# Optimization experiments

Measured on AMD Instinct MI355X. Metric: run time of the kernel, lower is better.

The kernel has to match this reference:

```python
import jax, jax.numpy as jnp
import numpy as np

B, T, M, D, N, K = 64, 128, 256, 256, 4, 2
TEMP = 8.0  # attention_temperature


def setup_inputs() -> dict:
    key = jax.random.key(0)
    ks = jax.random.split(key, 8)
    s = 0.05
    x = jax.random.normal(ks[0], (B, T, 8), jnp.float32)
    in_W = jax.random.normal(ks[1], (D, 8), jnp.float32) * s
    in_b = jnp.zeros((D,), jnp.float32)
    out_W = jax.random.normal(ks[2], (8, D), jnp.float32) * s
    out_b = jnp.zeros((8,), jnp.float32)
    proc_W = jax.random.normal(ks[3], (1, D, D), jnp.float32) * s  # depth-1 layers
    proc_b = jnp.zeros((1, D), jnp.float32)
    dest = jax.random.uniform(ks[4], (N, M), jnp.float32) * M  # pointer_destinations
    jg_W = jax.random.normal(ks[5], (N, 1, D), jnp.float32) * s
    jg_b = jnp.zeros((N, 1), jnp.float32)
    ctx_strength = jnp.full((N,), 0.2, jnp.float32)
    PHI = 1.618033988749895
    ph = []
    for n in range(N):
        phase_v = n * PHI
        row = []
        for h in range(1, 9):
            row += [np.sin(h * phase_v), np.cos(h * phase_v)]
        ph.append(row)
    phase = jnp.asarray(np.array(ph, dtype=np.float32))  # [N,16]
    # pointer init: being n uniform in [n*M/N, (n+1)*M/N)
    lo = jnp.arange(N, dtype=jnp.float32)[:, None] * (M / N)
    ptr_init = lo + jax.random.uniform(ks[6], (N, B), jnp.float32) * (M / N)
    return dict(x=x, in_W=in_W, in_b=in_b, out_W=out_W, out_b=out_b,
                proc_W=proc_W, proc_b=proc_b, dest=dest, jg_W=jg_W, jg_b=jg_b,
                ctx_strength=ctx_strength, phase=phase, ptr_init=ptr_init)


def _forward(x, in_W, in_b, out_W, out_b, proc_W, proc_b, dest, jg_W, jg_b,
             ctx_strength, phase, ptr_init):
    offsets = jnp.arange(-K, K + 1)           # [2K+1]
    half = M / 2.0
    phase_pad = jnp.pad(phase, ((0, 0), (0, D - phase.shape[1])))  # [N,D]
    brow = jnp.arange(B)[:, None]

    def step(carry, x_t):
        ring, hid, ptr = carry                # [B,M,D], [N,B,D], [N,B]
        inp = x_t @ in_W.T + in_b             # shared input_proj: [B,D]
        outs, nh, nptr = [], [], []
        for n in range(N):                    # small fixed swarm of beings
            p = ptr[n]                        # [B]
            base = jnp.clip(jnp.floor(p), 0, M - 1).astype(jnp.int32)
            idx = (base[:, None] + offsets) % M          # [B,2K+1]
            # circular distance from window cell to fractional pointer
            delta = jnp.mod(idx.astype(p.dtype) - p[:, None] + half, M) - half
            w = jax.nn.softmax(-(delta * delta) / TEMP, axis=1)  # [B,2K+1]
            neigh = jnp.take_along_axis(ring, idx[:, :, None], axis=1)  # [B,2K+1,D]
            ctx = jnp.sum(w[:, :, None] * neigh, axis=1)  # [B,D]
            comb = inp + jax.nn.sigmoid(ctx_strength[n]) * ctx + 0.1 * phase_pad[n]
            s_ = jnp.tanh(comb + hid[n])
            for l in range(proc_W.shape[0]):
                s_ = jnp.tanh(s_ @ proc_W[l].T + proc_b[l])
            # write the new hidden state back into the shared ring (gaussian-weighted)
            ring = ring.at[brow, idx].add(w[:, :, None] * s_[:, None, :])
            # straight-through hard jump gate
            jl = (s_ @ jg_W[n].T + jg_b[n])[:, 0]        # [B]
            pr = jax.nn.sigmoid(jl)
            hard = (pr > 0.5).astype(s_.dtype)
            g = pr + jax.lax.stop_gradient(hard - pr)
            dst = dest[n][base]                           # learned jump target
            walk = jnp.mod(p + 1.0, M)
            nptr.append(jnp.mod(g * dst + (1.0 - g) * walk, M))
            outs.append(s_ @ out_W.T + out_b)             # [B,8]
            nh.append(s_)
        combined = jnp.mean(jnp.stack(outs, 0), axis=0)   # mean combiner: [B,8]
        return (ring, jnp.stack(nh, 0), jnp.stack(nptr, 0)), combined

    ring0 = jnp.zeros((B, M, D), x.dtype)
    hid0 = jnp.zeros((N, B, D), x.dtype)
    _, ys = jax.lax.scan(step, (ring0, hid0, ptr_init), jnp.swapaxes(x, 0, 1))
    return jnp.swapaxes(ys, 0, 1)                         # [B,T,8]


def reference(x, in_W, in_b, out_W, out_b, proc_W, proc_b, dest, jg_W, jg_b,
              ctx_strength, phase, ptr_init):
    return _forward(x, in_W, in_b, out_W, out_b, proc_W, proc_b, dest, jg_W,
                    jg_b, ctx_strength, phase, ptr_init)
```

## Files before the change

### kernel.cpp

```cpp
#include <hip/hip_runtime.h>
#include <hip/hip_bf16.h>
#include <math.h>

#define BB 64
#define TT 128
#define MM 256
#define DD 256
#define NB 4

__global__ __launch_bounds__(1024, 1)
void swarm_kernel(const float* __restrict__ x,
                  const float* __restrict__ in_W,
                  const float* __restrict__ in_b,
                  const float* __restrict__ out_W,
                  const float* __restrict__ out_b,
                  const float* __restrict__ proc_W,
                  const float* __restrict__ proc_b,
                  const float* __restrict__ dest,
                  const float* __restrict__ jg_W,
                  const float* __restrict__ jg_b,
                  const float* __restrict__ ctx_strength,
                  const float* __restrict__ phase,
                  const float* __restrict__ ptr_init,
                  float* __restrict__ out,
                  float* __restrict__ ws)
{
  const int b    = blockIdx.x;
  const int tid  = threadIdx.x;
  const int wave = tid >> 6;
  const int lane = tid & 63;
  const int c    = tid >> 8;
  const int jj   = tid & 255;
  const bool j256 = (tid < 256);
  const int j = tid;

  float* __restrict__ ring = ws + (size_t)b * (MM * DD);

  __shared__ __align__(16) float s_lds[DD];
  __shared__ float part_lds[4 * DD];
  __shared__ float hid_lds[NB * DD];
  __shared__ float red_lds[4];
  __shared__ float red2_lds[32];
  __shared__ float ptr_lds[NB];
  __shared__ float cst_inWT[8 * DD];
  __shared__ float cst_inb[DD];
  __shared__ float cst_pb[DD];
  __shared__ float cst_jgW[NB * DD];
  __shared__ float cst_ph[NB * DD];
  __shared__ float cst_outW[8 * DD];
  __shared__ float cst_sig[NB];
  __shared__ float cst_jgb[NB];

  float Wreg[64];
  {
    const float4* src = (const float4*)(proc_W + (size_t)jj * DD + c * 64);
    #pragma unroll
    for (int q = 0; q < 16; ++q) {
      float4 v = src[q];
      Wreg[4*q+0] = v.x; Wreg[4*q+1] = v.y; Wreg[4*q+2] = v.z; Wreg[4*q+3] = v.w;
    }
  }

  for (int i = tid; i < 8 * DD; i += 1024) {
    int cc = i >> 8, jx = i & 255;
    cst_inWT[i] = in_W[jx * 8 + cc];
    cst_outW[i] = out_W[i];
  }
  {
    int i = tid;
    int n = i >> 8, jx = i & 255;
    cst_jgW[i] = jg_W[i];
    cst_ph[i]  = (jx < 16) ? 0.1f * phase[n * 16 + jx] : 0.f;
    hid_lds[i] = 0.f;
  }
  if (j256) { cst_inb[j] = in_b[j]; cst_pb[j] = proc_b[j]; }
  if (tid < NB) {
    cst_sig[tid] = 1.f / (1.f + expf(-ctx_strength[tid]));
    cst_jgb[tid] = jg_b[tid];
    ptr_lds[tid] = ptr_init[tid * BB + b];
  }

  {
    float4 z4 = make_float4(0.f, 0.f, 0.f, 0.f);
    float4* r4 = (float4*)ring;
    #pragma unroll
    for (int q = 0; q < (MM * DD / 4) / 1024; ++q)
      r4[q * 1024 + tid] = z4;
  }
  __syncthreads();

  for (int t = 0; t < TT; ++t) {
    float inp_r = 0.f;
    if (j256) {
      const float* xt = x + ((size_t)b * TT + t) * 8;
      float a = cst_inb[j];
      #pragma unroll
      for (int cc = 0; cc < 8; ++cc) a = fmaf(xt[cc], cst_inWT[cc * DD + j], a);
      inp_r = a;
    }
    float sacc = 0.f;

    #pragma unroll
    for (int n = 0; n < NB; ++n) {
      float p = 0.f, w5[5];
      int basei = 0;

      if (j256) {
        p = ptr_lds[n];
        basei = (int)floorf(p);
        if (basei < 0) basei = 0;
        if (basei > MM - 1) basei = MM - 1;
        float v5[5], mx = -1e30f;
        #pragma unroll
        for (int i = 0; i < 5; ++i) {
          int idx = (basei + i - 2 + MM) & (MM - 1);
          float d = (float)idx - p + 128.f;
          d -= 256.f * floorf(d * (1.f / 256.f));
          float del = d - 128.f;
          v5[i] = -(del * del) * 0.125f;
          mx = fmaxf(mx, v5[i]);
        }
        float se = 0.f;
        #pragma unroll
        for (int i = 0; i < 5; ++i) { w5[i] = expf(v5[i] - mx); se += w5[i]; }
        float inv = 1.f / se;
        float ctx = 0.f;
        #pragma unroll
        for (int i = 0; i < 5; ++i) {
          w5[i] *= inv;
          int idx = (basei + i - 2 + MM) & (MM - 1);
          ctx = fmaf(w5[i], ring[idx * DD + j], ctx);
        }
        float comb = inp_r + cst_sig[n] * ctx + cst_ph[n * DD + j];
        s_lds[j] = tanhf(comb + hid_lds[n * DD + j]);
      }
      __syncthreads();

      {
        float a0 = 0.f, a1 = 0.f, a2 = 0.f, a3 = 0.f;
        const float4* s4 = (const float4*)(s_lds + c * 64);
        #pragma unroll
        for (int q = 0; q < 16; ++q) {
          float4 sv = s4[q];
          a0 = fmaf(Wreg[4*q+0], sv.x, a0);
          a1 = fmaf(Wreg[4*q+1], sv.y, a1);
          a2 = fmaf(Wreg[4*q+2], sv.z, a2);
          a3 = fmaf(Wreg[4*q+3], sv.w, a3);
        }
        part_lds[c * DD + jj] = (a0 + a1) + (a2 + a3);
      }
      __syncthreads();

      if (j256) {
        float sum = ((part_lds[j] + part_lds[DD + j]) +
                     (part_lds[2 * DD + j] + part_lds[3 * DD + j])) + cst_pb[j];
        float s2 = tanhf(sum);
        hid_lds[n * DD + j] = s2;
        sacc += s2;
        #pragma unroll
        for (int i = 0; i < 5; ++i) {
          int idx = (basei + i - 2 + MM) & (MM - 1);
          float* rp = ring + idx * DD + j;
          *rp = *rp + w5[i] * s2;
        }
        float v = s2 * cst_jgW[n * DD + j];
        #pragma unroll
        for (int off = 32; off > 0; off >>= 1) v += __shfl_down(v, off, 64);
        if (lane == 0) red_lds[wave] = v;
      }
      __syncthreads();

      if (j256) {
        float jl = ((red_lds[0] + red_lds[1]) + (red_lds[2] + red_lds[3])) + cst_jgb[n];
        if (tid == 0) {
          float dstv = dest[n * MM + basei];
          float walk = p + 1.f;
          if (walk >= 256.f) walk -= 256.f;
          ptr_lds[n] = (jl > 0.f) ? dstv : walk;
        }
      }
    }

    if (j256) {
      #pragma unroll
      for (int o = 0; o < 8; ++o) {
        float v = sacc * cst_outW[o * DD + j];
        #pragma unroll
        for (int off = 32; off > 0; off >>= 1) v += __shfl_down(v, off, 64);
        if (lane == 0) red2_lds[o * 4 + wave] = v;
      }
    }
    __syncthreads();
    if (tid < 8) {
      float s = (red2_lds[tid * 4 + 0] + red2_lds[tid * 4 + 1]) +
                (red2_lds[tid * 4 + 2] + red2_lds[tid * 4 + 3]);
      out[((size_t)b * TT + t) * 8 + tid] = out_b[tid] + 0.25f * s;
    }
    __syncthreads();
  }
}

extern "C" void kernel_launch(void* const* d_in, const int* in_sizes, int n_in,
                              void* d_out, int out_size, void* d_ws, size_t ws_size,
                              hipStream_t stream) {
  const float* x        = (const float*)d_in[0];
  const float* in_W     = (const float*)d_in[1];
  const float* in_b     = (const float*)d_in[2];
  const float* out_W    = (const float*)d_in[3];
  const float* out_b    = (const float*)d_in[4];
  const float* proc_W   = (const float*)d_in[5];
  const float* proc_b   = (const float*)d_in[6];
  const float* dest     = (const float*)d_in[7];
  const float* jg_W     = (const float*)d_in[8];
  const float* jg_b     = (const float*)d_in[9];
  const float* ctx_s    = (const float*)d_in[10];
  const float* phase    = (const float*)d_in[11];
  const float* ptr_init = (const float*)d_in[12];
  float* outp = (float*)d_out;
  float* ws   = (float*)d_ws;

  hipLaunchKernelGGL(swarm_kernel, dim3(BB), dim3(1024), 0, stream,
                     x, in_W, in_b, out_W, out_b, proc_W, proc_b, dest,
                     jg_W, jg_b, ctx_s, phase, ptr_init, outp, ws);
}
```

Baseline: 1.455 ms.

## Defer pointer update across beings to drop per-step barriers

The jump-gate reduction result and pointer update for each being are moved into the next being's phase, with red_lds double-buffered. This removes one block barrier per being and the trailing barrier per timestep. The dest lookup is prefetched early. Barriers become a custom lgkmcnt-only wait plus s_barrier, which skips waiting on outstanding global memory operations. Launch bounds now use a waves-per-EU attribute, and an empty asm keeps the weight array in VGPRs. Correctness depends on each thread touching only its own ring column, so global writes need no cross-thread ordering.

After: 1.480 ms. Within noise of the previous version (+1.7%).

```diff
diff --git a/kernel.cpp b/kernel.cpp
--- a/kernel.cpp
+++ b/kernel.cpp
@@ -8,7 +8,13 @@
 #define DD 256
 #define NB 4
 
-__global__ __launch_bounds__(1024, 1)
+#define BARL()                                          \
+  do {                                                  \
+    asm volatile("s_waitcnt lgkmcnt(0)" ::: "memory");  \
+    __builtin_amdgcn_s_barrier();                       \
+  } while (0)
+
+__global__ __launch_bounds__(1024) __attribute__((amdgpu_waves_per_eu(4, 4)))
 void swarm_kernel(const float* __restrict__ x,
                   const float* __restrict__ in_W,
                   const float* __restrict__ in_b,
@@ -39,7 +45,7 @@
   __shared__ __align__(16) float s_lds[DD];
   __shared__ float part_lds[4 * DD];
   __shared__ float hid_lds[NB * DD];
-  __shared__ float red_lds[4];
+  __shared__ float red_lds[8];
   __shared__ float red2_lds[32];
   __shared__ float ptr_lds[NB];
   __shared__ float cst_inWT[8 * DD];
@@ -60,6 +66,8 @@
       Wreg[4*q+0] = v.x; Wreg[4*q+1] = v.y; Wreg[4*q+2] = v.z; Wreg[4*q+3] = v.w;
     }
   }
+  #pragma unroll
+  for (int q = 0; q < 64; ++q) asm volatile("" : "+v"(Wreg[q]));
 
   for (int i = tid; i < 8 * DD; i += 1024) {
     int cc = i >> 8, jx = i & 255;
@@ -88,6 +96,8 @@
       r4[q * 1024 + tid] = z4;
   }
   __syncthreads();
+
+  float prevp = 0.f, dst_prev = 0.f, dst_cur = 0.f;
 
   for (int t = 0; t < TT; ++t) {
     float inp_r = 0.f;
@@ -110,6 +120,7 @@
         basei = (int)floorf(p);
         if (basei < 0) basei = 0;
         if (basei > MM - 1) basei = MM - 1;
+        if (tid == 0) dst_cur = dest[n * MM + basei];
         float v5[5], mx = -1e30f;
         #pragma unroll
         for (int i = 0; i < 5; ++i) {
@@ -134,22 +145,43 @@
         float comb = inp_r + cst_sig[n] * ctx + cst_ph[n * DD + j];
         s_lds[j] = tanhf(comb + hid_lds[n * DD + j]);
       }
-      __syncthreads();
+      BARL();
+
+      if (n > 0 && tid == 0) {
+        int slot = (n - 1) & 1;
+        float jl = ((red_lds[slot * 4 + 0] + red_lds[slot * 4 + 1]) +
+                    (red_lds[slot * 4 + 2] + red_lds[slot * 4 + 3])) + cst_jgb[n - 1];
+        float walk = prevp + 1.f;
+        if (walk >= 256.f) walk -= 256.f;
+        ptr_lds[n - 1] = (jl > 0.f) ? dst_prev : walk;
+      }
 
       {
         float a0 = 0.f, a1 = 0.f, a2 = 0.f, a3 = 0.f;
-        const float4* s4 = (const float4*)(s_lds + c * 64);
-        #pragma unroll
-        for (int q = 0; q < 16; ++q) {
-          float4 sv = s4[q];
-          a0 = fmaf(Wreg[4*q+0], sv.x, a0);
-          a1 = fmaf(Wreg[4*q+1], sv.y, a1);
-          a2 = fmaf(Wreg[4*q+2], sv.z, a2);
-          a3 = fmaf(Wreg[4*q+3], sv.w, a3);
-        }
-        part_lds[c * DD + jj] = (a0 + a1) + (a2 + a3);
-      }
-      __syncthreads();
+        const float4* s4 = (const float4*)(s_lds + (c << 6));
+        #pragma unroll
+        for (int g = 0; g < 4; ++g) {
+          float4 sv0 = s4[4*g+0], sv1 = s4[4*g+1], sv2 = s4[4*g+2], sv3 = s4[4*g+3];
+          a0 = fmaf(Wreg[16*g+ 0], sv0.x, a0);
+          a1 = fmaf(Wreg[16*g+ 1], sv0.y, a1);
+          a2 = fmaf(Wreg[16*g+ 2], sv0.z, a2);
+          a3 = fmaf(Wreg[16*g+ 3], sv0.w, a3);
+          a0 = fmaf(Wreg[16*g+ 4], sv1.x, a0);
+          a1 = fmaf(Wreg[16*g+ 5], sv1.y, a1);
+          a2 = fmaf(Wreg[16*g+ 6], sv1.z, a2);
+          a3 = fmaf(Wreg[16*g+ 7], sv1.w, a3);
+          a0 = fmaf(Wreg[16*g+ 8], sv2.x, a0);
+          a1 = fmaf(Wreg[16*g+ 9], sv2.y, a1);
+          a2 = fmaf(Wreg[16*g+10], sv2.z, a2);
+          a3 = fmaf(Wreg[16*g+11], sv2.w, a3);
+          a0 = fmaf(Wreg[16*g+12], sv3.x, a0);
+          a1 = fmaf(Wreg[16*g+13], sv3.y, a1);
+          a2 = fmaf(Wreg[16*g+14], sv3.z, a2);
+          a3 = fmaf(Wreg[16*g+15], sv3.w, a3);
+        }
+        part_lds[(c << 8) + jj] = (a0 + a1) + (a2 + a3);
+      }
+      BARL();
 
       if (j256) {
         float sum = ((part_lds[j] + part_lds[DD + j]) +
@@ -166,19 +198,9 @@
         float v = s2 * cst_jgW[n * DD + j];
         #pragma unroll
         for (int off = 32; off > 0; off >>= 1) v += __shfl_down(v, off, 64);
-        if (lane == 0) red_lds[wave] = v;
-      }
-      __syncthreads();
-
-      if (j256) {
-        float jl = ((red_lds[0] + red_lds[1]) + (red_lds[2] + red_lds[3])) + cst_jgb[n];
-        if (tid == 0) {
-          float dstv = dest[n * MM + basei];
-          float walk = p + 1.f;
-          if (walk >= 256.f) walk -= 256.f;
-          ptr_lds[n] = (jl > 0.f) ? dstv : walk;
-        }
-      }
+        if (lane == 0) red_lds[(n & 1) * 4 + wave] = v;
+      }
+      prevp = p; dst_prev = dst_cur;
     }
 
     if (j256) {
@@ -190,13 +212,19 @@
         if (lane == 0) red2_lds[o * 4 + wave] = v;
       }
     }
-    __syncthreads();
+    BARL();
+
+    if (tid == 0) {
+      float jl = ((red_lds[4] + red_lds[5]) + (red_lds[6] + red_lds[7])) + cst_jgb[3];
+      float walk = prevp + 1.f;
+      if (walk >= 256.f) walk -= 256.f;
+      ptr_lds[3] = (jl > 0.f) ? dst_prev : walk;
+    }
     if (tid < 8) {
       float s = (red2_lds[tid * 4 + 0] + red2_lds[tid * 4 + 1]) +
                 (red2_lds[tid * 4 + 2] + red2_lds[tid * 4 + 3]);
       out[((size_t)b * TT + t) * 8 + tid] = out_b[tid] + 0.25f * s;
     }
-    __syncthreads();
   }
 }
 
```
